# Kernel tuning notes

Measured on AMD Instinct MI355X. Metric: run time of the kernel, lower is better.

Reference implementation:

```python
import jax, jax.numpy as jnp
import numpy as np
import math

N = 100000
E = 1600000
D_IN = 128
H = 128
OUT = 10
NEG = -1e30


def setup_inputs() -> dict:
    key = jax.random.key(0)
    ks = jax.random.split(key, 24)
    def lin(k, fi, fo):
        s = 1.0 / np.sqrt(fi)
        return jax.random.uniform(k, (fi, fo), jnp.float32, -s, s)
    inp = {
        'x': jax.random.normal(ks[0], (N, D_IN), jnp.float32),
        'edge_index': jax.random.randint(ks[1], (2, E), 0, N, jnp.int64),
        'W1': lin(ks[2], D_IN, H), 'b1': jnp.zeros((H,), jnp.float32),
        'ws1': lin(ks[3], H, 1), 'bs1': jnp.zeros((1,), jnp.float32),
        'W2': lin(ks[4], H, H), 'b2': jnp.zeros((H,), jnp.float32),
        'ws2': lin(ks[5], H, 1), 'bs2': jnp.zeros((1,), jnp.float32),
        'W3': lin(ks[6], H, H), 'b3': jnp.zeros((H,), jnp.float32),
        'ws3': lin(ks[7], H, 1), 'bs3': jnp.zeros((1,), jnp.float32),
        'M1': lin(ks[8], 2 * H, H), 'bm1': jnp.zeros((H,), jnp.float32),
        'M2': lin(ks[9], H, H // 2), 'bm2': jnp.zeros((H // 2,), jnp.float32),
        'M3': lin(ks[10], H // 2, OUT), 'bm3': jnp.zeros((OUT,), jnp.float32),
    }
    return inp


def _gcn(x, W, b, src, dst, node_mask, edge_mask):
    # GCNConv with self-loops: deg[i] = self_loop + in_degree over valid edges
    deg = node_mask + jax.ops.segment_sum(edge_mask, dst, num_segments=N)
    dinv = jnp.where(deg > 0, jax.lax.rsqrt(deg), 0.0)
    coef = edge_mask * dinv[src] * dinv[dst]            # [E]
    agg = jax.ops.segment_sum(coef[:, None] * x[src], dst, num_segments=N)
    agg = agg + (node_mask * dinv * dinv)[:, None] * x   # self-loop term
    return (agg @ W + b) * node_mask[:, None]


def _sag_pool(x, ws, bs, src, dst, node_mask, edge_mask, k):
    # score via 1-dim GCNConv, top-k (ratio 0.5) select, tanh gating, edge filtering
    score = _gcn(x, ws, bs, src, dst, node_mask, edge_mask)[:, 0]
    _, idx = jax.lax.top_k(jnp.where(node_mask > 0, score, -jnp.inf), k)
    new_mask = jnp.zeros((N,), x.dtype).at[idx].set(1.0)
    x_new = x * jnp.tanh(score)[:, None] * new_mask[:, None]
    e_new = edge_mask * new_mask[src] * new_mask[dst]
    return x_new, new_mask, e_new


def _readout(x, mask, k):
    mean = jnp.sum(x * mask[:, None], axis=0) / k
    mx = jnp.max(jnp.where(mask[:, None] > 0, x, NEG), axis=0)
    return jnp.concatenate([mean, mx])[None, :]   # [1, 2H]


def reference(x, edge_index, W1, b1, ws1, bs1, W2, b2, ws2, bs2, W3, b3, ws3, bs3, M1, bm1, M2, bm2, M3, bm3):
    src, dst = edge_index[0], edge_index[1]
    nm0 = jnp.ones((N,), jnp.float32)
    em0 = jnp.ones((E,), jnp.float32)
    k1 = math.ceil(0.5 * N)
    k2 = math.ceil(0.5 * k1)
    k3 = math.ceil(0.5 * k2)

    h1 = jax.nn.relu(_gcn(x, W1, b1, src, dst, nm0, em0))
    x1, nm1, em1 = _sag_pool(h1, ws1, bs1, src, dst, nm0, em0, k1)
    r1 = _readout(x1, nm1, k1)

    h2 = jax.nn.relu(_gcn(x1, W2, b2, src, dst, nm1, em1))
    x2, nm2, em2 = _sag_pool(h2, ws2, bs2, src, dst, nm1, em1, k2)
    r2 = _readout(x2, nm2, k2)

    h3 = jax.nn.relu(_gcn(x2, W3, b3, src, dst, nm2, em2))
    x3, nm3, em3 = _sag_pool(h3, ws3, bs3, src, dst, nm2, em2, k3)
    r3 = _readout(x3, nm3, k3)

    readout = r1 + r2 + r3                              # [1, 2H]
    y = jax.nn.relu(readout @ M1 + bm1)
    y = jax.nn.relu(y @ M2 + bm2)
    y = y @ M3 + bm3
    return jax.nn.log_softmax(y, axis=1)
```

## Files before the change

kernel.cpp:

```cpp
#include <hip/hip_runtime.h>
#include <cstdint>
#include <cstddef>

#define NN 100000
#define EE 1600000
#define HH 128
#define NB_N 391
#define NBKT 391
#define CAP 5120


static __device__ __forceinline__ unsigned fsort_(float f){
  unsigned u = __float_as_uint(f);
  return (u & 0x80000000u) ? ~u : (u | 0x80000000u);
}
static __device__ __forceinline__ unsigned bfbits_(float f){
  unsigned u = __float_as_uint(f);
  return (u + 0x7FFFu + ((u >> 16) & 1u)) >> 16;
}
static __device__ __forceinline__ unsigned bfpack_(float f0, float f1){
  return bfbits_(f0) | (bfbits_(f1) << 16);
}
static __device__ __forceinline__ float bflo_(unsigned u){ return __uint_as_float(u << 16); }
static __device__ __forceinline__ float bfhi_(unsigned u){ return __uint_as_float(u & 0xFFFF0000u); }

__global__ void k_edgeflag(const int* __restrict__ ei, unsigned* __restrict__ state,
                           unsigned* __restrict__ bktcnt){
  int t = threadIdx.x;
  if(t < 64){
    int v = ei[2*t + 1];
    unsigned long long m = __ballot(v != 0);
    if(t == 0) state[8] = (m == 0ull) ? 1u : 0u;
  }
  if(t >= 12 && t < 24) state[t] = 0u;
  for(int j=t; j<NBKT; j+=256) bktcnt[j] = 0u;
}

__global__ __launch_bounds__(256) void k_binA(const int* __restrict__ ei,
                     const unsigned* __restrict__ state,
                     unsigned* __restrict__ bktcnt, unsigned* __restrict__ staging){
  __shared__ unsigned lcnt[NBKT];
  __shared__ unsigned lloc[NBKT];
  int t = threadIdx.x;
  for(int j=t; j<NBKT; j+=256){ lcnt[j] = 0u; lloc[j] = 0u; }
  bool i64 = (state[8] != 0u);
  int e0 = blockIdx.x*4096;
  int es[16], ed[16];
  #pragma unroll
  for(int k=0;k<16;k++){
    int e = e0 + k*256 + t;
    int s = -1, d = 0;
    if(e < EE){
      if(i64){ s = ei[2*e]; d = ei[2*EE + 2*e]; }
      else   { s = ei[e];   d = ei[EE + e]; }
    }
    es[k] = s; ed[k] = d;
  }
  __syncthreads();
  #pragma unroll
  for(int k=0;k<16;k++){
    if(es[k] >= 0) atomicAdd(&lcnt[ed[k]>>8], 1u);
  }
  __syncthreads();
  for(int j=t; j<NBKT; j+=256){
    unsigned c = lcnt[j];
    lcnt[j] = c ? atomicAdd(&bktcnt[j], c) : 0u;
  }
  __syncthreads();
  #pragma unroll
  for(int k=0;k<16;k++){
    if(es[k] >= 0){
      int b = ed[k] >> 8;
      unsigned off = lcnt[b] + atomicAdd(&lloc[b], 1u);
      if(off < CAP)
        staging[(unsigned)b*CAP + off] = (unsigned)es[k] | (((unsigned)(ed[k] & 255)) << 17);
    }
  }
}

__global__ __launch_bounds__(256) void k_binB(const unsigned* __restrict__ staging,
                     const unsigned* __restrict__ bktcnt,
                     int* __restrict__ rs, int* __restrict__ rl, int* __restrict__ col,
                     float* __restrict__ dinv){
  __shared__ unsigned hist[256];
  __shared__ unsigned pref[256];
  __shared__ unsigned lfill[256];
  __shared__ unsigned baseSh;
  int t = threadIdx.x;
  int b = blockIdx.x;
  unsigned s = 0;
  for(int j=t; j<b; j+=256) s += bktcnt[j];
  pref[t] = s;
  __syncthreads();
  for(int off=128; off>0; off>>=1){
    if(t < off) pref[t] += pref[t+off];
    __syncthreads();
  }
  if(t == 0) baseSh = pref[0];
  __syncthreads();
  unsigned base = baseSh;
  unsigned cnt = bktcnt[b]; if(cnt > CAP) cnt = CAP;
  hist[t] = 0u; lfill[t] = 0u;
  __syncthreads();
  const unsigned* st = staging + (unsigned)b*CAP;
  for(unsigned i=t; i<cnt; i+=256) atomicAdd(&hist[st[i]>>17], 1u);
  __syncthreads();
  unsigned h = hist[t];
  pref[t] = h;
  __syncthreads();
  for(int off=1; off<256; off<<=1){
    unsigned u = (t >= off) ? pref[t-off] : 0u;
    __syncthreads();
    pref[t] += u;
    __syncthreads();
  }
  unsigned excl = pref[t] - h;
  int node = b*256 + t;
  if(node < NN){
    rs[node] = (int)(base + excl);
    rl[node] = (int)h;
    dinv[node] = rsqrtf(1.f + (float)h);
  }
  __syncthreads();
  pref[t] = excl;
  __syncthreads();
  for(unsigned i=t; i<cnt; i+=256){
    unsigned w = st[i];
    unsigned dl = w >> 17;
    unsigned pos = base + pref[dl] + atomicAdd(&lfill[dl], 1u);
    col[pos] = (int)(w & 0x1FFFFu);
  }
}

template<int MODE>
__global__ __launch_bounds__(256) void k_gemm(const void* __restrict__ xin_,
        const float* __restrict__ gate, const int* __restrict__ alist, int nrows,
        const float* __restrict__ W, unsigned short* __restrict__ y16){
  __shared__ float sX[16][68];
  __shared__ float sW[16][64];
  __shared__ int rowid[64];
  __shared__ float rowg[64];
  int row0 = blockIdx.x*64, col0 = blockIdx.y*64;
  int t = threadIdx.x;
  if(t < 64){
    int gr = row0 + t;
    int node = -1; float gg = 0.f;
    if(gr < nrows){
      node = MODE ? alist[gr] : gr;
      gg = MODE ? gate[node] : 1.f;
    }
    rowid[t] = node; rowg[t] = gg;
  }
  __syncthreads();
  int tx = t & 15, ty = t >> 4;
  float acc[4][4] = {{0.f}};
  const float* xf = (const float*)xin_;
  const unsigned short* xh = (const unsigned short*)xin_;
  for(int kb=0; kb<HH; kb+=16){
    #pragma unroll
    for(int j=0;j<4;j++){
      int r = (t>>4) + j*16;
      int k = t & 15;
      int node = rowid[r];
      float v = 0.f;
      if(node >= 0){
        if(MODE) v = __uint_as_float(((unsigned)xh[(size_t)node*HH + kb + k]) << 16) * rowg[r];
        else     v = xf[(size_t)node*HH + kb + k];
      }
      sX[k][r] = v;
    }
    #pragma unroll
    for(int j=0;j<4;j++){
      int k = (t>>6) + j*4;
      int c = t & 63;
      sW[k][c] = W[(size_t)(kb+k)*HH + col0 + c];
    }
    __syncthreads();
    #pragma unroll
    for(int k=0;k<16;k++){
      float4 xv = *(const float4*)&sX[k][ty*4];
      float4 wv = *(const float4*)&sW[k][tx*4];
      float xs[4] = {xv.x, xv.y, xv.z, xv.w};
      float wsv[4] = {wv.x, wv.y, wv.z, wv.w};
      #pragma unroll
      for(int a=0;a<4;a++)
        #pragma unroll
        for(int b=0;b<4;b++)
          acc[a][b] += xs[a]*wsv[b];
    }
    __syncthreads();
  }
  #pragma unroll
  for(int a=0;a<4;a++){
    int node = rowid[ty*4 + a];
    if(node >= 0){
      uint2 o;
      o.x = bfpack_(acc[a][0], acc[a][1]);
      o.y = bfpack_(acc[a][2], acc[a][3]);
      *(uint2*)&y16[(size_t)node*HH + col0 + tx*4] = o;
    }
  }
}

template<int LIST>
__global__ __launch_bounds__(256) void k_agg(const unsigned short* __restrict__ y16,
        const float* __restrict__ dinv,
        const int* __restrict__ rs, const int* __restrict__ rl,
        const int* __restrict__ col, const int* __restrict__ alist,
        const float* __restrict__ bias, const float* __restrict__ wsc,
        unsigned short* __restrict__ h16, float* __restrict__ p,
        unsigned* __restrict__ hist){
  if(blockIdx.x < 512) hist[blockIdx.x*256 + threadIdx.x] = 0u;
  int w = (blockIdx.x*256 + threadIdx.x) >> 6;
  int lane = threadIdx.x & 63;
  int g = lane >> 4, c = lane & 15;
  int node = LIST ? alist[w] : w;
  float di = dinv[node];
  int e0 = rs[node], len = rl[node];
  float a0=0,a1=0,a2=0,a3=0,a4=0,a5=0,a6=0,a7=0;
  int i = g;
  for(; i + 4 < len; i += 8){
    int s0 = col[e0+i], s1 = col[e0+i+4];
    float d0 = dinv[s0], d1 = dinv[s1];
    uint4 v0 = ((const uint4*)(y16 + (size_t)s0*HH))[c];
    uint4 v1 = ((const uint4*)(y16 + (size_t)s1*HH))[c];
    a0 += d0*bflo_(v0.x) + d1*bflo_(v1.x);
    a1 += d0*bfhi_(v0.x) + d1*bfhi_(v1.x);
    a2 += d0*bflo_(v0.y) + d1*bflo_(v1.y);
    a3 += d0*bfhi_(v0.y) + d1*bfhi_(v1.y);
    a4 += d0*bflo_(v0.z) + d1*bflo_(v1.z);
    a5 += d0*bfhi_(v0.z) + d1*bfhi_(v1.z);
    a6 += d0*bflo_(v0.w) + d1*bflo_(v1.w);
    a7 += d0*bfhi_(v0.w) + d1*bfhi_(v1.w);
  }
  if(i < len){
    int s = col[e0+i];
    float ds = dinv[s];
    uint4 v = ((const uint4*)(y16 + (size_t)s*HH))[c];
    a0 += ds*bflo_(v.x); a1 += ds*bfhi_(v.x);
    a2 += ds*bflo_(v.y); a3 += ds*bfhi_(v.y);
    a4 += ds*bflo_(v.z); a5 += ds*bfhi_(v.z);
    a6 += ds*bflo_(v.w); a7 += ds*bfhi_(v.w);
  }
  a0 += __shfl_xor(a0,16,64); a0 += __shfl_xor(a0,32,64);
  a1 += __shfl_xor(a1,16,64); a1 += __shfl_xor(a1,32,64);
  a2 += __shfl_xor(a2,16,64); a2 += __shfl_xor(a2,32,64);
  a3 += __shfl_xor(a3,16,64); a3 += __shfl_xor(a3,32,64);
  a4 += __shfl_xor(a4,16,64); a4 += __shfl_xor(a4,32,64);
  a5 += __shfl_xor(a5,16,64); a5 += __shfl_xor(a5,32,64);
  a6 += __shfl_xor(a6,16,64); a6 += __shfl_xor(a6,32,64);
  a7 += __shfl_xor(a7,16,64); a7 += __shfl_xor(a7,32,64);
  uint4 sv = ((const uint4*)(y16 + (size_t)node*HH))[c];
  const float4* b4 = (const float4*)bias;
  float4 bb0 = b4[2*c], bb1 = b4[2*c+1];
  float d2 = di*di;
  float o0 = fmaxf(di*a0 + d2*bflo_(sv.x) + bb0.x, 0.f);
  float o1 = fmaxf(di*a1 + d2*bfhi_(sv.x) + bb0.y, 0.f);
  float o2 = fmaxf(di*a2 + d2*bflo_(sv.y) + bb0.z, 0.f);
  float o3 = fmaxf(di*a3 + d2*bfhi_(sv.y) + bb0.w, 0.f);
  float o4 = fmaxf(di*a4 + d2*bflo_(sv.z) + bb1.x, 0.f);
  float o5 = fmaxf(di*a5 + d2*bfhi_(sv.z) + bb1.y, 0.f);
  float o6 = fmaxf(di*a6 + d2*bflo_(sv.w) + bb1.z, 0.f);
  float o7 = fmaxf(di*a7 + d2*bfhi_(sv.w) + bb1.w, 0.f);
  if(g == 0){
    uint4 o;
    o.x = bfpack_(o0,o1); o.y = bfpack_(o2,o3);
    o.z = bfpack_(o4,o5); o.w = bfpack_(o6,o7);
    ((uint4*)(h16 + (size_t)node*HH))[c] = o;
  }
  const float4* w4 = (const float4*)wsc;
  float4 w0 = w4[2*c], w1 = w4[2*c+1];
  float pp = o0*w0.x + o1*w0.y + o2*w0.z + o3*w0.w
           + o4*w1.x + o5*w1.y + o6*w1.z + o7*w1.w;
  pp += __shfl_xor(pp, 1, 64);
  pp += __shfl_xor(pp, 2, 64);
  pp += __shfl_xor(pp, 4, 64);
  pp += __shfl_xor(pp, 8, 64);
  if(lane == 0) p[node] = pp;
}

template<int LIST>
__global__ void k_score(const float* __restrict__ p, const float* __restrict__ dinv,
                        const int* __restrict__ rs, const int* __restrict__ rl,
                        const int* __restrict__ col, const int* __restrict__ alist, int n,
                        const float* __restrict__ bs, float* __restrict__ score,
                        unsigned* __restrict__ key, unsigned* __restrict__ hist){
  int w = blockIdx.x*256 + threadIdx.x;
  if(w >= n) return;
  int i = LIST ? alist[w] : w;
  float di = dinv[i];
  float s = 0.f;
  int e0 = rs[i], len = rl[i];
  for(int e=e0; e<e0+len; e++){
    int cidx = col[e];
    s += dinv[cidx]*p[cidx];
  }
  float sc = di*s + di*di*p[i] + bs[0];
  score[i] = sc;
  unsigned kv = fsort_(sc);
  key[i] = kv;
  atomicAdd(&hist[kv>>16], 1u);
}

__global__ void k_hist_lo(const unsigned* __restrict__ key, const unsigned* __restrict__ state,
                          unsigned* __restrict__ histB){
  int i = blockIdx.x*256 + threadIdx.x;
  if(i < NN){
    unsigned kv = key[i];
    if((kv >> 16) == state[0]) atomicAdd(&histB[kv & 0xFFFFu], 1u);
  }
}
__global__ void k_pick(const unsigned* __restrict__ hist, unsigned* __restrict__ state,
                       int k_in, int mode){
  __shared__ unsigned csum[256];
  int t = threadIdx.x;
  const uint4* h4 = (const uint4*)(hist + t*256);
  unsigned s = 0;
  for(int j=0;j<64;j++){ uint4 v = h4[j]; s += v.x+v.y+v.z+v.w; }
  csum[t] = s;
  __syncthreads();
  for(int off=1; off<256; off<<=1){
    unsigned v = (t+off < 256) ? csum[t+off] : 0u;
    __syncthreads();
    csum[t] += v;
    __syncthreads();
  }
  unsigned k = (mode == 0) ? (unsigned)k_in : state[1];
  unsigned above = csum[t] - s;
  if(above < k && above + s >= k){
    unsigned run = above;
    for(int j=255; j>=0; j--){
      unsigned c = hist[t*256+j];
      if(run + c >= k){
        if(mode == 0){ state[0] = (unsigned)(t*256+j); state[1] = k - run; }
        else { state[2] = (state[0] << 16) | (unsigned)(t*256+j); state[3] = k - run; }
        break;
      }
      run += c;
    }
  }
}

__global__ __launch_bounds__(256) void k_maskCR(unsigned* __restrict__ key,
        const float* __restrict__ score, const unsigned* __restrict__ state,
        const unsigned short* __restrict__ h16,
        unsigned char* __restrict__ selm, float* __restrict__ gate,
        int* __restrict__ alist_out, unsigned* __restrict__ acounter,
        float* __restrict__ rpart, int slotbase){
  __shared__ int wcnt[4];
  __shared__ int priorSh;
  __shared__ int redi[256];
  __shared__ float gl[256];
  __shared__ unsigned char slf[256];
  __shared__ float4 red[256];
  __shared__ float out2[256];
  int t = threadIdx.x;
  int i = blockIdx.x*256 + t;
  unsigned T = state[2];
  int trem = (int)state[3];
  unsigned kv = (i < NN) ? key[i] : 0u;
  bool match = (kv == T);
  unsigned long long m = __ballot(match);
  int lane = t & 63, wid = t >> 6;
  if(lane == 0) wcnt[wid] = __popcll(m);
  if(t == 0) priorSh = 0;
  __syncthreads();
  int hasMatch = wcnt[0] | wcnt[1] | wcnt[2] | wcnt[3];
  int bbase = blockIdx.x*256;
  if(hasMatch){
    int cm = 0;
    for(int j = t*4; j < bbase; j += 1024){
      uint4 kk = *(const uint4*)&key[j];
      cm += (kk.x==T) + (kk.y==T) + (kk.z==T) + (kk.w==T);
    }
    redi[t] = cm;
    __syncthreads();
    for(int off=128; off>0; off>>=1){
      if(t < off) redi[t] += redi[t+off];
      __syncthreads();
    }
    if(t == 0) priorSh = redi[0];
    __syncthreads();
  }
  int pre = 0;
  for(int w=0; w<wid; w++) pre += wcnt[w];
  int lrank = __popcll(m & ((1ull << lane) - 1ull));
  int rank = priorSh + pre + lrank;
  bool sel = (kv > T) || (match && rank < trem);
  float gg = sel ? tanhf(score[i]) : 0.f;
  gl[t] = gg;
  slf[t] = sel ? 1 : 0;
  if(i < NN){
    selm[i] = sel ? 1 : 0;
    gate[i] = gg;
    if(!sel) key[i] = 0u;
  }
  unsigned long long sm = __ballot(sel);
  unsigned abase = 0;
  if(lane == 0) abase = atomicAdd(acounter, (unsigned)__popcll(sm));
  abase = (unsigned)__shfl((int)abase, 0, 64);
  if(sel) alist_out[abase + __popcll(sm & ((1ull << lane) - 1ull))] = i;
  __syncthreads();
  int ch = t & 15;
  int slot = t >> 4;
  float mm[8] = {0,0,0,0,0,0,0,0};
  float MM[8] = {-1e30f,-1e30f,-1e30f,-1e30f,-1e30f,-1e30f,-1e30f,-1e30f};
  for(int itr=0; itr<16; itr++){
    int nl = slot + itr*16;
    int node = bbase + nl;
    if(node < NN && slf[nl]){
      float g = gl[nl];
      uint4 v = ((const uint4*)(h16 + (size_t)node*HH))[ch];
      float x0 = g*bflo_(v.x), x1 = g*bfhi_(v.x);
      float x2 = g*bflo_(v.y), x3 = g*bfhi_(v.y);
      float x4 = g*bflo_(v.z), x5 = g*bfhi_(v.z);
      float x6 = g*bflo_(v.w), x7 = g*bfhi_(v.w);
      mm[0]+=x0; mm[1]+=x1; mm[2]+=x2; mm[3]+=x3;
      mm[4]+=x4; mm[5]+=x5; mm[6]+=x6; mm[7]+=x7;
      MM[0]=fmaxf(MM[0],x0); MM[1]=fmaxf(MM[1],x1); MM[2]=fmaxf(MM[2],x2); MM[3]=fmaxf(MM[3],x3);
      MM[4]=fmaxf(MM[4],x4); MM[5]=fmaxf(MM[5],x5); MM[6]=fmaxf(MM[6],x6); MM[7]=fmaxf(MM[7],x7);
    }
  }
  #pragma unroll
  for(int half=0; half<2; half++){
    red[t] = make_float4(mm[half*4+0],mm[half*4+1],mm[half*4+2],mm[half*4+3]);
    __syncthreads();
    if(t < 16){
      float4 sacc = red[t];
      for(int j=1;j<16;j++){
        float4 o = red[t + 16*j];
        sacc.x += o.x; sacc.y += o.y; sacc.z += o.z; sacc.w += o.w;
      }
      int d = t*8 + half*4;
      out2[d+0] = sacc.x; out2[d+1] = sacc.y; out2[d+2] = sacc.z; out2[d+3] = sacc.w;
    }
    __syncthreads();
    red[t] = make_float4(MM[half*4+0],MM[half*4+1],MM[half*4+2],MM[half*4+3]);
    __syncthreads();
    if(t < 16){
      float4 sacc = red[t];
      for(int j=1;j<16;j++){
        float4 o = red[t + 16*j];
        sacc.x = fmaxf(sacc.x,o.x); sacc.y = fmaxf(sacc.y,o.y);
        sacc.z = fmaxf(sacc.z,o.z); sacc.w = fmaxf(sacc.w,o.w);
      }
      int d = 128 + t*8 + half*4;
      out2[d+0] = sacc.x; out2[d+1] = sacc.y; out2[d+2] = sacc.z; out2[d+3] = sacc.w;
    }
    __syncthreads();
  }
  rpart[(size_t)(slotbase + blockIdx.x)*256 + t] = out2[t];
}

__global__ __launch_bounds__(256) void k_compact(const int* __restrict__ alist, int n,
        const unsigned char* __restrict__ selm,
        const int* __restrict__ rs_old, const int* __restrict__ rl_old,
        const int* __restrict__ col_old,
        int* __restrict__ rs_new, int* __restrict__ rl_new, int* __restrict__ col_new,
        float* __restrict__ dinv, unsigned* __restrict__ ecnt){
  __shared__ unsigned gcnt[16];
  __shared__ unsigned gbase[16];
  __shared__ unsigned blkbase;
  int t = threadIdx.x;
  int g = t >> 4, lane = t & 15;
  int gsh = ((t >> 4) & 3) * 16;
  int idx = blockIdx.x*16 + g;
  int node = -1, e0 = 0, len = 0;
  if(idx < n){ node = alist[idx]; e0 = rs_old[node]; len = rl_old[node]; }
  int cnt = 0;
  for(int i=lane; i<len; i+=16) cnt += selm[col_old[e0+i]];
  cnt += __shfl_xor(cnt,1,64); cnt += __shfl_xor(cnt,2,64);
  cnt += __shfl_xor(cnt,4,64); cnt += __shfl_xor(cnt,8,64);
  if(lane == 0) gcnt[g] = (node >= 0) ? (unsigned)cnt : 0u;
  __syncthreads();
  if(t == 0){
    unsigned s = 0;
    for(int j=0;j<16;j++){ gbase[j] = s; s += gcnt[j]; }
    blkbase = s ? atomicAdd(ecnt, s) : 0u;
  }
  __syncthreads();
  unsigned base = blkbase + gbase[g];
  if(node >= 0 && lane == 0){
    rs_new[node] = (int)base;
    rl_new[node] = cnt;
    dinv[node] = rsqrtf(1.f + (float)cnt);
  }
  int pos = (int)base;
  for(int i0=0; i0<len; i0+=16){
    int i = i0 + lane;
    bool keep = false; int s = 0;
    if(i < len){ s = col_old[e0+i]; keep = (selm[s] != 0); }
    unsigned long long b = __ballot(keep);
    unsigned gb = (unsigned)((b >> gsh) & 0xFFFFull);
    int rank = __popc(gb & ((1u << lane) - 1u));
    if(keep) col_new[pos + rank] = s;
    pos += __popc(gb);
  }
}

__global__ void k_mlp(const float* __restrict__ rpart,
                      const float* __restrict__ M1, const float* __restrict__ bm1,
                      const float* __restrict__ M2, const float* __restrict__ bm2,
                      const float* __restrict__ M3, const float* __restrict__ bm3,
                      float* __restrict__ out){
  __shared__ float R[256];
  __shared__ float y1[128];
  __shared__ float y2[64];
  __shared__ float y3[16];
  int t = threadIdx.x;
  const float kinv[3] = {1.f/50000.f, 1.f/25000.f, 1.f/12500.f};
  if(t < 128){
    float acc = 0.f;
    for(int l=0; l<3; l++){
      float s0=0.f,s1=0.f,s2=0.f,s3=0.f;
      int base = l*NB_N;
      int j = 0;
      for(; j+3 < NB_N; j += 4){
        s0 += rpart[(size_t)(base+j  )*256 + t];
        s1 += rpart[(size_t)(base+j+1)*256 + t];
        s2 += rpart[(size_t)(base+j+2)*256 + t];
        s3 += rpart[(size_t)(base+j+3)*256 + t];
      }
      for(; j < NB_N; j++) s0 += rpart[(size_t)(base+j)*256 + t];
      acc += ((s0+s1)+(s2+s3)) * kinv[l];
    }
    R[t] = acc;
  } else {
    float acc = 0.f;
    for(int l=0; l<3; l++){
      float m0=-1e30f,m1=-1e30f,m2=-1e30f,m3=-1e30f;
      int base = l*NB_N;
      int j = 0;
      for(; j+3 < NB_N; j += 4){
        m0 = fmaxf(m0, rpart[(size_t)(base+j  )*256 + t]);
        m1 = fmaxf(m1, rpart[(size_t)(base+j+1)*256 + t]);
        m2 = fmaxf(m2, rpart[(size_t)(base+j+2)*256 + t]);
        m3 = fmaxf(m3, rpart[(size_t)(base+j+3)*256 + t]);
      }
      for(; j < NB_N; j++) m0 = fmaxf(m0, rpart[(size_t)(base+j)*256 + t]);
      acc += fmaxf(fmaxf(m0,m1), fmaxf(m2,m3));
    }
    R[t] = acc;
  }
  __syncthreads();
  if(t < 128){
    float a = bm1[t];
    for(int d=0; d<256; d++) a += R[d]*M1[d*128+t];
    y1[t] = fmaxf(a, 0.f);
  }
  __syncthreads();
  if(t < 64){
    float a = bm2[t];
    for(int d=0; d<128; d++) a += y1[d]*M2[d*64+t];
    y2[t] = fmaxf(a, 0.f);
  }
  __syncthreads();
  if(t < 10){
    float a = bm3[t];
    for(int d=0; d<64; d++) a += y2[d]*M3[d*10+t];
    y3[t] = a;
  }
  __syncthreads();
  if(t == 0){
    float mx = -1e30f;
    for(int o=0;o<10;o++) mx = fmaxf(mx, y3[o]);
    float s = 0.f;
    for(int o=0;o<10;o++) s += expf(y3[o]-mx);
    float ls = logf(s);
    for(int o=0;o<10;o++) out[o] = y3[o] - mx - ls;
  }
}

extern "C" void kernel_launch(void* const* d_in, const int* in_sizes, int n_in,
                              void* d_out, int out_size, void* d_ws, size_t ws_size,
                              hipStream_t stream){
  (void)in_sizes; (void)n_in; (void)out_size; (void)ws_size;
  const float* x  = (const float*)d_in[0];
  const int*   ei = (const int*)d_in[1];
  const float* W[3]   = {(const float*)d_in[2],  (const float*)d_in[6],  (const float*)d_in[10]};
  const float* bb[3]  = {(const float*)d_in[3],  (const float*)d_in[7],  (const float*)d_in[11]};
  const float* wsc[3] = {(const float*)d_in[4],  (const float*)d_in[8],  (const float*)d_in[12]};
  const float* bsc[3] = {(const float*)d_in[5],  (const float*)d_in[9],  (const float*)d_in[13]};
  const float* M1  = (const float*)d_in[14];
  const float* bm1 = (const float*)d_in[15];
  const float* M2  = (const float*)d_in[16];
  const float* bm2 = (const float*)d_in[17];
  const float* M3  = (const float*)d_in[18];
  const float* bm3 = (const float*)d_in[19];
  float* out = (float*)d_out;

  char* base = (char*)d_ws;
  size_t off = 0;
  auto alloc = [&](size_t bytes)->char*{
    char* ptr = base + off;
    off += (bytes + 511) & ~(size_t)511;
    return ptr;
  };
  unsigned short* y16  = (unsigned short*)alloc((size_t)NN*HH*2);
  unsigned short* h16  = (unsigned short*)alloc((size_t)NN*HH*2);
  int*      col0      = (int*)     alloc((size_t)EE*4);
  int*      col1      = (int*)     alloc((size_t)EE*4);
  int*      col2      = (int*)     alloc((size_t)EE*4);
  unsigned* staging   = (unsigned*)alloc((size_t)NBKT*CAP*4);
  int*      rs0       = (int*)     alloc((size_t)NN*4);
  int*      rl0       = (int*)     alloc((size_t)NN*4);
  int*      rs1       = (int*)     alloc((size_t)NN*4);
  int*      rl1       = (int*)     alloc((size_t)NN*4);
  int*      rs2       = (int*)     alloc((size_t)NN*4);
  int*      rl2       = (int*)     alloc((size_t)NN*4);
  float*    dinv      = (float*)   alloc((size_t)NN*4);
  float*    pbuf      = (float*)   alloc((size_t)NN*4);
  float*    score     = (float*)   alloc((size_t)NN*4);
  float*    gate      = (float*)   alloc((size_t)NN*4);
  unsigned* key       = (unsigned*)alloc((size_t)NN*4);
  unsigned char* selm = (unsigned char*)alloc((size_t)NN);
  int*      alistA    = (int*)     alloc((size_t)50000*4);
  int*      alistB    = (int*)     alloc((size_t)25000*4);
  unsigned* hist      = (unsigned*)alloc((size_t)2*65536*4);
  unsigned* bktcnt    = (unsigned*)alloc((size_t)(NBKT+1)*4);
  unsigned* state     = (unsigned*)alloc(256);
  float*    rpart     = (float*)   alloc((size_t)3*NB_N*256*4);

  k_edgeflag<<<1,256,0,stream>>>(ei, state, bktcnt);
  k_binA<<<NBKT,256,0,stream>>>(ei, state, bktcnt, staging);
  k_binB<<<NBKT,256,0,stream>>>(staging, bktcnt, rs0, rl0, col0, dinv);

  k_gemm<0><<<dim3(1563,2),256,0,stream>>>(x, nullptr, nullptr, NN, W[0], y16);
  k_agg<0><<<25000,256,0,stream>>>(y16, dinv, rs0, rl0, col0, nullptr, bb[0], wsc[0], h16, pbuf, hist);
  k_score<0><<<NB_N,256,0,stream>>>(pbuf, dinv, rs0, rl0, col0, nullptr, NN, bsc[0], score, key, hist);
  k_pick<<<1,256,0,stream>>>(hist, state, 50000, 0);
  k_hist_lo<<<NB_N,256,0,stream>>>(key, state, hist + 65536);
  k_pick<<<1,256,0,stream>>>(hist + 65536, state, 0, 1);
  k_maskCR<<<NB_N,256,0,stream>>>(key, score, state, h16, selm, gate, alistA, state+12, rpart, 0);
  k_compact<<<3125,256,0,stream>>>(alistA, 50000, selm, rs0, rl0, col0, rs1, rl1, col1, dinv, state+16);

  k_gemm<1><<<dim3(782,2),256,0,stream>>>(h16, gate, alistA, 50000, W[1], y16);
  k_agg<1><<<12500,256,0,stream>>>(y16, dinv, rs1, rl1, col1, alistA, bb[1], wsc[1], h16, pbuf, hist);
  k_score<1><<<196,256,0,stream>>>(pbuf, dinv, rs1, rl1, col1, alistA, 50000, bsc[1], score, key, hist);
  k_pick<<<1,256,0,stream>>>(hist, state, 25000, 0);
  k_hist_lo<<<NB_N,256,0,stream>>>(key, state, hist + 65536);
  k_pick<<<1,256,0,stream>>>(hist + 65536, state, 0, 1);
  k_maskCR<<<NB_N,256,0,stream>>>(key, score, state, h16, selm, gate, alistB, state+13, rpart, NB_N);
  k_compact<<<1563,256,0,stream>>>(alistB, 25000, selm, rs1, rl1, col1, rs2, rl2, col2, dinv, state+17);

  k_gemm<1><<<dim3(391,2),256,0,stream>>>(h16, gate, alistB, 25000, W[2], y16);
  k_agg<1><<<6250,256,0,stream>>>(y16, dinv, rs2, rl2, col2, alistB, bb[2], wsc[2], h16, pbuf, hist);
  k_score<1><<<98,256,0,stream>>>(pbuf, dinv, rs2, rl2, col2, alistB, 25000, bsc[2], score, key, hist);
  k_pick<<<1,256,0,stream>>>(hist, state, 12500, 0);
  k_hist_lo<<<NB_N,256,0,stream>>>(key, state, hist + 65536);
  k_pick<<<1,256,0,stream>>>(hist + 65536, state, 0, 1);
  k_maskCR<<<NB_N,256,0,stream>>>(key, score, state, h16, selm, gate, alistA, state+14, rpart, 2*NB_N);

  k_mlp<<<1,256,0,stream>>>(rpart, M1, bm1, M2, bm2, M3, bm3, out);
}
```

Measured before the change: 803.9 us.

## Fold source-degree normalization into GEMM output and simplify aggregation loops

```diff
diff --git a/kernel.cpp b/kernel.cpp
--- a/kernel.cpp
+++ b/kernel.cpp
@@ -9,6 +9,8 @@
 #define NBKT 391
 #define CAP 5120
 
+
+typedef float f32x2 __attribute__((ext_vector_type(2)));
 
 static __device__ __forceinline__ unsigned fsort_(float f){
   unsigned u = __float_as_uint(f);
@@ -134,7 +136,8 @@
 
 template<int MODE>
 __global__ __launch_bounds__(256) void k_gemm(const void* __restrict__ xin_,
-        const float* __restrict__ gate, const int* __restrict__ alist, int nrows,
+        const float* __restrict__ gate, const float* __restrict__ dinv,
+        const int* __restrict__ alist, int nrows,
         const float* __restrict__ W, unsigned short* __restrict__ y16){
   __shared__ float sX[16][68];
   __shared__ float sW[16][64];
@@ -144,12 +147,12 @@
   int t = threadIdx.x;
   if(t < 64){
     int gr = row0 + t;
-    int node = -1; float gg = 0.f;
+    int node = -1; float sc = 0.f;
     if(gr < nrows){
       node = MODE ? alist[gr] : gr;
-      gg = MODE ? gate[node] : 1.f;
-    }
-    rowid[t] = node; rowg[t] = gg;
+      sc = MODE ? dinv[node]*gate[node] : dinv[node];
+    }
+    rowid[t] = node; rowg[t] = sc;
   }
   __syncthreads();
   int tx = t & 15, ty = t >> 4;
@@ -164,7 +167,7 @@
       int node = rowid[r];
       float v = 0.f;
       if(node >= 0){
-        if(MODE) v = __uint_as_float(((unsigned)xh[(size_t)node*HH + kb + k]) << 16) * rowg[r];
+        if(MODE) v = __uint_as_float(((unsigned)xh[(size_t)node*HH + kb + k]) << 16);
         else     v = xf[(size_t)node*HH + kb + k];
       }
       sX[k][r] = v;
@@ -192,15 +195,25 @@
   }
   #pragma unroll
   for(int a=0;a<4;a++){
-    int node = rowid[ty*4 + a];
+    int r = ty*4 + a;
+    int node = rowid[r];
     if(node >= 0){
+      float s = rowg[r];
       uint2 o;
-      o.x = bfpack_(acc[a][0], acc[a][1]);
-      o.y = bfpack_(acc[a][2], acc[a][3]);
+      o.x = bfpack_(s*acc[a][0], s*acc[a][1]);
+      o.y = bfpack_(s*acc[a][2], s*acc[a][3]);
       *(uint2*)&y16[(size_t)node*HH + col0 + tx*4] = o;
     }
   }
 }
+
+#define ACCQ(V) do{ \
+  f32x2 t0,t1,t2,t3; \
+  t0.x=__uint_as_float((V).x<<16); t0.y=__uint_as_float((V).x&0xFFFF0000u); \
+  t1.x=__uint_as_float((V).y<<16); t1.y=__uint_as_float((V).y&0xFFFF0000u); \
+  t2.x=__uint_as_float((V).z<<16); t2.y=__uint_as_float((V).z&0xFFFF0000u); \
+  t3.x=__uint_as_float((V).w<<16); t3.y=__uint_as_float((V).w&0xFFFF0000u); \
+  a01+=t0; a23+=t1; a45+=t2; a67+=t3; }while(0)
 
 template<int LIST>
 __global__ __launch_bounds__(256) void k_agg(const unsigned short* __restrict__ y16,
@@ -217,31 +230,28 @@
   int node = LIST ? alist[w] : w;
   float di = dinv[node];
   int e0 = rs[node], len = rl[node];
-  float a0=0,a1=0,a2=0,a3=0,a4=0,a5=0,a6=0,a7=0;
-  int i = g;
-  for(; i + 4 < len; i += 8){
-    int s0 = col[e0+i], s1 = col[e0+i+4];
-    float d0 = dinv[s0], d1 = dinv[s1];
-    uint4 v0 = ((const uint4*)(y16 + (size_t)s0*HH))[c];
-    uint4 v1 = ((const uint4*)(y16 + (size_t)s1*HH))[c];
-    a0 += d0*bflo_(v0.x) + d1*bflo_(v1.x);
-    a1 += d0*bfhi_(v0.x) + d1*bfhi_(v1.x);
-    a2 += d0*bflo_(v0.y) + d1*bflo_(v1.y);
-    a3 += d0*bfhi_(v0.y) + d1*bfhi_(v1.y);
-    a4 += d0*bflo_(v0.z) + d1*bflo_(v1.z);
-    a5 += d0*bfhi_(v0.z) + d1*bfhi_(v1.z);
-    a6 += d0*bflo_(v0.w) + d1*bflo_(v1.w);
-    a7 += d0*bfhi_(v0.w) + d1*bfhi_(v1.w);
-  }
-  if(i < len){
-    int s = col[e0+i];
-    float ds = dinv[s];
-    uint4 v = ((const uint4*)(y16 + (size_t)s*HH))[c];
-    a0 += ds*bflo_(v.x); a1 += ds*bfhi_(v.x);
-    a2 += ds*bflo_(v.y); a3 += ds*bfhi_(v.y);
-    a4 += ds*bflo_(v.z); a5 += ds*bfhi_(v.z);
-    a6 += ds*bflo_(v.w); a7 += ds*bfhi_(v.w);
-  }
+  const char* yb = (const char*)y16;
+  unsigned lc16 = (unsigned)(c << 4);
+  int chunk = (len + 3) >> 2;
+  int ib = g*chunk;
+  int ie = ib + chunk; if(ie > len) ie = len;
+  f32x2 a01 = {0.f,0.f}, a23 = {0.f,0.f}, a45 = {0.f,0.f}, a67 = {0.f,0.f};
+  const int* ce = col + e0;
+  int i = ib;
+  for(; i+3 < ie; i += 4){
+    int c0 = ce[i], c1 = ce[i+1], c2 = ce[i+2], c3 = ce[i+3];
+    uint4 v0 = *(const uint4*)(yb + (((unsigned)c0<<8) | lc16));
+    uint4 v1 = *(const uint4*)(yb + (((unsigned)c1<<8) | lc16));
+    uint4 v2 = *(const uint4*)(yb + (((unsigned)c2<<8) | lc16));
+    uint4 v3 = *(const uint4*)(yb + (((unsigned)c3<<8) | lc16));
+    ACCQ(v0); ACCQ(v1); ACCQ(v2); ACCQ(v3);
+  }
+  for(; i < ie; i++){
+    int c0 = ce[i];
+    uint4 v0 = *(const uint4*)(yb + (((unsigned)c0<<8) | lc16));
+    ACCQ(v0);
+  }
+  float a0=a01.x, a1=a01.y, a2=a23.x, a3=a23.y, a4=a45.x, a5=a45.y, a6=a67.x, a7=a67.y;
   a0 += __shfl_xor(a0,16,64); a0 += __shfl_xor(a0,32,64);
   a1 += __shfl_xor(a1,16,64); a1 += __shfl_xor(a1,32,64);
   a2 += __shfl_xor(a2,16,64); a2 += __shfl_xor(a2,32,64);
@@ -250,18 +260,17 @@
   a5 += __shfl_xor(a5,16,64); a5 += __shfl_xor(a5,32,64);
   a6 += __shfl_xor(a6,16,64); a6 += __shfl_xor(a6,32,64);
   a7 += __shfl_xor(a7,16,64); a7 += __shfl_xor(a7,32,64);
-  uint4 sv = ((const uint4*)(y16 + (size_t)node*HH))[c];
+  uint4 sv = *(const uint4*)(yb + (((unsigned)node<<8) | lc16));
   const float4* b4 = (const float4*)bias;
   float4 bb0 = b4[2*c], bb1 = b4[2*c+1];
-  float d2 = di*di;
-  float o0 = fmaxf(di*a0 + d2*bflo_(sv.x) + bb0.x, 0.f);
-  float o1 = fmaxf(di*a1 + d2*bfhi_(sv.x) + bb0.y, 0.f);
-  float o2 = fmaxf(di*a2 + d2*bflo_(sv.y) + bb0.z, 0.f);
-  float o3 = fmaxf(di*a3 + d2*bfhi_(sv.y) + bb0.w, 0.f);
-  float o4 = fmaxf(di*a4 + d2*bflo_(sv.z) + bb1.x, 0.f);
-  float o5 = fmaxf(di*a5 + d2*bfhi_(sv.z) + bb1.y, 0.f);
-  float o6 = fmaxf(di*a6 + d2*bflo_(sv.w) + bb1.z, 0.f);
-  float o7 = fmaxf(di*a7 + d2*bfhi_(sv.w) + bb1.w, 0.f);
+  float o0 = fmaxf(fmaf(di, a0 + bflo_(sv.x), bb0.x), 0.f);
+  float o1 = fmaxf(fmaf(di, a1 + bfhi_(sv.x), bb0.y), 0.f);
+  float o2 = fmaxf(fmaf(di, a2 + bflo_(sv.y), bb0.z), 0.f);
+  float o3 = fmaxf(fmaf(di, a3 + bfhi_(sv.y), bb0.w), 0.f);
+  float o4 = fmaxf(fmaf(di, a4 + bflo_(sv.z), bb1.x), 0.f);
+  float o5 = fmaxf(fmaf(di, a5 + bfhi_(sv.z), bb1.y), 0.f);
+  float o6 = fmaxf(fmaf(di, a6 + bflo_(sv.w), bb1.z), 0.f);
+  float o7 = fmaxf(fmaf(di, a7 + bfhi_(sv.w), bb1.w), 0.f);
   if(g == 0){
     uint4 o;
     o.x = bfpack_(o0,o1); o.y = bfpack_(o2,o3);
@@ -276,7 +285,7 @@
   pp += __shfl_xor(pp, 2, 64);
   pp += __shfl_xor(pp, 4, 64);
   pp += __shfl_xor(pp, 8, 64);
-  if(lane == 0) p[node] = pp;
+  if(lane == 0) p[node] = di*pp;
 }
 
 template<int LIST>
@@ -291,11 +300,14 @@
   float di = dinv[i];
   float s = 0.f;
   int e0 = rs[i], len = rl[i];
-  for(int e=e0; e<e0+len; e++){
-    int cidx = col[e];
-    s += dinv[cidx]*p[cidx];
-  }
-  float sc = di*s + di*di*p[i] + bs[0];
+  const int* ce = col + e0;
+  int e = 0;
+  for(; e+3 < len; e += 4){
+    int c0 = ce[e], c1 = ce[e+1], c2 = ce[e+2], c3 = ce[e+3];
+    s += (p[c0] + p[c1]) + (p[c2] + p[c3]);
+  }
+  for(; e < len; e++) s += p[ce[e]];
+  float sc = di*(s + p[i]) + bs[0];
   score[i] = sc;
   unsigned kv = fsort_(sc);
   key[i] = kv;
@@ -625,7 +637,7 @@
   k_binA<<<NBKT,256,0,stream>>>(ei, state, bktcnt, staging);
   k_binB<<<NBKT,256,0,stream>>>(staging, bktcnt, rs0, rl0, col0, dinv);
 
-  k_gemm<0><<<dim3(1563,2),256,0,stream>>>(x, nullptr, nullptr, NN, W[0], y16);
+  k_gemm<0><<<dim3(1563,2),256,0,stream>>>(x, nullptr, dinv, nullptr, NN, W[0], y16);
   k_agg<0><<<25000,256,0,stream>>>(y16, dinv, rs0, rl0, col0, nullptr, bb[0], wsc[0], h16, pbuf, hist);
   k_score<0><<<NB_N,256,0,stream>>>(pbuf, dinv, rs0, rl0, col0, nullptr, NN, bsc[0], score, key, hist);
   k_pick<<<1,256,0,stream>>>(hist, state, 50000, 0);
@@ -634,7 +646,7 @@
   k_maskCR<<<NB_N,256,0,stream>>>(key, score, state, h16, selm, gate, alistA, state+12, rpart, 0);
   k_compact<<<3125,256,0,stream>>>(alistA, 50000, selm, rs0, rl0, col0, rs1, rl1, col1, dinv, state+16);
 
-  k_gemm<1><<<dim3(782,2),256,0,stream>>>(h16, gate, alistA, 50000, W[1], y16);
+  k_gemm<1><<<dim3(782,2),256,0,stream>>>(h16, gate, dinv, alistA, 50000, W[1], y16);
   k_agg<1><<<12500,256,0,stream>>>(y16, dinv, rs1, rl1, col1, alistA, bb[1], wsc[1], h16, pbuf, hist);
   k_score<1><<<196,256,0,stream>>>(pbuf, dinv, rs1, rl1, col1, alistA, 50000, bsc[1], score, key, hist);
   k_pick<<<1,256,0,stream>>>(hist, state, 25000, 0);
@@ -643,7 +655,7 @@
   k_maskCR<<<NB_N,256,0,stream>>>(key, score, state, h16, selm, gate, alistB, state+13, rpart, NB_N);
   k_compact<<<1563,256,0,stream>>>(alistB, 25000, selm, rs1, rl1, col1, rs2, rl2, col2, dinv, state+17);
 
-  k_gemm<1><<<dim3(391,2),256,0,stream>>>(h16, gate, alistB, 25000, W[2], y16);
+  k_gemm<1><<<dim3(391,2),256,0,stream>>>(h16, gate, dinv, alistB, 25000, W[2], y16);
   k_agg<1><<<6250,256,0,stream>>>(y16, dinv, rs2, rl2, col2, alistB, bb[2], wsc[2], h16, pbuf, hist);
   k_score<1><<<98,256,0,stream>>>(pbuf, dinv, rs2, rl2, col2, alistB, 25000, bsc[2], score, key, hist);
   k_pick<<<1,256,0,stream>>>(hist, state, 12500, 0);
```

After: 782.9 us. -2.6%, faster.
